# Kernel optimization log

Measured on AMD Instinct MI355X. Metric: run time of the kernel, lower is better.

Reference implementation:

```python
import jax, jax.numpy as jnp
import numpy as np

NODE_TYPE_SIZE = 9      # common.NodeType.SIZE in MeshGraphNets
N_NODES = 1_000_000
N_CELLS = 2_000_000


def setup_inputs() -> dict:
    key = jax.random.key(0)
    k1, k2, k3, k4, k5 = jax.random.split(key, 5)
    world_pos = jax.random.normal(k1, (1, N_NODES, 3), dtype=jnp.float32)
    prev_world_pos = world_pos + 0.01 * jax.random.normal(k2, (1, N_NODES, 3), dtype=jnp.float32)
    mesh_pos = jax.random.normal(k3, (1, N_NODES, 3), dtype=jnp.float32)
    node_type = jax.random.randint(k4, (1, N_NODES, 1), 0, NODE_TYPE_SIZE, dtype=jnp.int64)
    # random triangles with guaranteed-distinct vertices (avoids degenerate
    # zero-length edges, matching real meshes where triangle corners differ)
    base = jax.random.randint(k5, (N_CELLS, 1), 0, N_NODES, dtype=jnp.int64)
    cells = jnp.mod(base + jnp.arange(3, dtype=jnp.int64)[None, :], N_NODES)[None]
    return {
        'world_pos': world_pos,
        'prev_world_pos': prev_world_pos,
        'mesh_pos': mesh_pos,
        'node_type': node_type,
        'cells': cells,
    }


def _triangles_to_edges(cells):
    # cells: [F, 3] -> bidirectional directed edge list [2 * 3F]
    a, b, c = cells[:, 0], cells[:, 1], cells[:, 2]
    u = jnp.concatenate([a, b, c])  # edge endpoints (a,b),(b,c),(c,a)
    v = jnp.concatenate([b, c, a])
    senders = jnp.concatenate([u, v])
    receivers = jnp.concatenate([v, u])
    return senders, receivers


def reference(world_pos, prev_world_pos, mesh_pos, node_type, cells):
    # squeeze the leading batch dim of 1, as the torch module does
    world_pos = jnp.squeeze(world_pos, 0)          # [N, 3]
    prev_world_pos = jnp.squeeze(prev_world_pos, 0)
    mesh_pos = jnp.squeeze(mesh_pos, 0)
    node_type = jnp.squeeze(node_type, 0)          # [N, 1]
    cells = jnp.squeeze(cells, 0)                  # [F, 3]

    velocity = world_pos - prev_world_pos                                   # [N, 3]
    nt_onehot = jax.nn.one_hot(node_type[:, 0], NODE_TYPE_SIZE,
                               dtype=world_pos.dtype)                        # [N, 9]
    node_features = jnp.concatenate([velocity, nt_onehot], axis=-1)          # [N, 12]

    senders, receivers = _triangles_to_edges(cells)                          # [E]
    rel_world = world_pos[senders] - world_pos[receivers]                    # [E, 3]
    rel_mesh = mesh_pos[senders] - mesh_pos[receivers]                       # [E, 3]
    edge_features = jnp.concatenate([
        rel_world,
        jnp.linalg.norm(rel_world, axis=-1, keepdims=True),
        rel_mesh,
        jnp.linalg.norm(rel_mesh, axis=-1, keepdims=True),
    ], axis=-1)                                                              # [E, 7]
    return node_features, edge_features
```

## Files before the change

### kernel.cpp

```cpp
#include <hip/hip_runtime.h>

__global__ void node_kernel(const float* __restrict__ w,
                            const float* __restrict__ p,
                            const int* __restrict__ nt,
                            float4* __restrict__ out, int n_nodes) {
    int i = blockIdx.x * blockDim.x + threadIdx.x;
    if (i >= n_nodes) return;
    size_t b = 3 * (size_t)i;
    float v0 = w[b + 0] - p[b + 0];
    float v1 = w[b + 1] - p[b + 1];
    float v2 = w[b + 2] - p[b + 2];
    int t = nt[i];
    float4 f0 = make_float4(v0, v1, v2, t == 0 ? 1.f : 0.f);
    float4 f1 = make_float4(t == 1 ? 1.f : 0.f, t == 2 ? 1.f : 0.f,
                            t == 3 ? 1.f : 0.f, t == 4 ? 1.f : 0.f);
    float4 f2 = make_float4(t == 5 ? 1.f : 0.f, t == 6 ? 1.f : 0.f,
                            t == 7 ? 1.f : 0.f, t == 8 ? 1.f : 0.f);
    float4* dst = out + 3 * (size_t)i;
    dst[0] = f0;
    dst[1] = f1;
    dst[2] = f2;
}

__device__ __forceinline__ void load3(const float* __restrict__ base, int n,
                                      float& x, float& y, float& z) {
    const float* q = base + 3 * (size_t)n;
    x = q[0]; y = q[1]; z = q[2];
}

__device__ __forceinline__ void emit(float4* __restrict__ ef, size_t e_fwd, size_t e_rev,
                                     float rwx, float rwy, float rwz,
                                     float rmx, float rmy, float rmz) {
    float nw = sqrtf(rwx * rwx + rwy * rwy + rwz * rwz);
    float nm = sqrtf(rmx * rmx + rmy * rmy + rmz * rmz);
    ef[2 * e_fwd + 0] = make_float4(rwx, rwy, rwz, nw);
    ef[2 * e_fwd + 1] = make_float4(rmx, rmy, rmz, nm);
    ef[2 * e_rev + 0] = make_float4(-rwx, -rwy, -rwz, nw);
    ef[2 * e_rev + 1] = make_float4(-rmx, -rmy, -rmz, nm);
}

__global__ void edge_kernel(const float* __restrict__ world,
                            const float* __restrict__ mesh,
                            const int* __restrict__ cells,
                            float4* __restrict__ ef, int n_cells) {
    int c = blockIdx.x * blockDim.x + threadIdx.x;
    if (c >= n_cells) return;
    size_t cb = 3 * (size_t)c;
    int ia = cells[cb + 0];
    int ib = cells[cb + 1];
    int ic = cells[cb + 2];

    float wax, way, waz, wbx, wby, wbz, wcx, wcy, wcz;
    load3(world, ia, wax, way, waz);
    load3(world, ib, wbx, wby, wbz);
    load3(world, ic, wcx, wcy, wcz);
    float max_, may_, maz_, mbx_, mby_, mbz_, mcx_, mcy_, mcz_;
    load3(mesh, ia, max_, may_, maz_);
    load3(mesh, ib, mbx_, mby_, mbz_);
    load3(mesh, ic, mcx_, mcy_, mcz_);

    size_t NC = (size_t)n_cells;
    size_t e = (size_t)c;
    emit(ef, e,          e + 3 * NC,
         wax - wbx, way - wby, waz - wbz,
         max_ - mbx_, may_ - mby_, maz_ - mbz_);
    emit(ef, e + NC,     e + 4 * NC,
         wbx - wcx, wby - wcy, wbz - wcz,
         mbx_ - mcx_, mby_ - mcy_, mbz_ - mcz_);
    emit(ef, e + 2 * NC, e + 5 * NC,
         wcx - wax, wcy - way, wcz - waz,
         mcx_ - max_, mcy_ - may_, mcz_ - maz_);
}

extern "C" void kernel_launch(void* const* d_in, const int* in_sizes, int n_in,
                              void* d_out, int out_size, void* d_ws, size_t ws_size,
                              hipStream_t stream) {
    const float* world = (const float*)d_in[0];
    const float* prev  = (const float*)d_in[1];
    const float* mesh  = (const float*)d_in[2];
    const int* ntype   = (const int*)d_in[3];
    const int* cells   = (const int*)d_in[4];
    int n_nodes = in_sizes[0] / 3;
    int n_cells = in_sizes[4] / 3;

    float* out = (float*)d_out;
    float4* nf = (float4*)out;
    float4* ef = (float4*)(out + (size_t)n_nodes * 12);

    dim3 blk(256);
    dim3 g_node((n_nodes + 255) / 256);
    dim3 g_edge((n_cells + 255) / 256);
    node_kernel<<<g_node, blk, 0, stream>>>(world, prev, ntype, nf, n_nodes);
    edge_kernel<<<g_edge, blk, 0, stream>>>(world, mesh, cells, ef, n_cells);
}
```

Before: 598.7 us.

## Fuse node and edge kernels into one launch with vectorized nontemporal stores

Merges the node and edge kernels into a single grid, with block ranges split between edge and node work, so one launch replaces two and the tail of one can overlap the other. Each edge thread handles two cells and reads cell indices as int2. Each node thread handles four nodes using float4 loads of positions and an int4 load of types. All outputs are written with nontemporal 16-byte stores. It adds more registers per thread, fewer threads in flight for the gather-bound edge work, and tail-handling branches.

Result: slower. 960.0 us (+60.3%).

```diff
diff --git a/kernel.cpp b/kernel.cpp
--- a/kernel.cpp
+++ b/kernel.cpp
@@ -1,75 +1,151 @@
 #include <hip/hip_runtime.h>
 
-__global__ void node_kernel(const float* __restrict__ w,
-                            const float* __restrict__ p,
-                            const int* __restrict__ nt,
-                            float4* __restrict__ out, int n_nodes) {
-    int i = blockIdx.x * blockDim.x + threadIdx.x;
-    if (i >= n_nodes) return;
-    size_t b = 3 * (size_t)i;
-    float v0 = w[b + 0] - p[b + 0];
-    float v1 = w[b + 1] - p[b + 1];
-    float v2 = w[b + 2] - p[b + 2];
-    int t = nt[i];
-    float4 f0 = make_float4(v0, v1, v2, t == 0 ? 1.f : 0.f);
-    float4 f1 = make_float4(t == 1 ? 1.f : 0.f, t == 2 ? 1.f : 0.f,
-                            t == 3 ? 1.f : 0.f, t == 4 ? 1.f : 0.f);
-    float4 f2 = make_float4(t == 5 ? 1.f : 0.f, t == 6 ? 1.f : 0.f,
-                            t == 7 ? 1.f : 0.f, t == 8 ? 1.f : 0.f);
-    float4* dst = out + 3 * (size_t)i;
-    dst[0] = f0;
-    dst[1] = f1;
-    dst[2] = f2;
+typedef float f4 __attribute__((ext_vector_type(4)));
+
+struct F3 { float x, y, z; };
+
+__device__ __forceinline__ F3 ldf3(const float* __restrict__ p) {
+    F3 r;
+    __builtin_memcpy(&r, p, sizeof(F3));
+    return r;
+}
+__device__ __forceinline__ F3 sub3(F3 a, F3 b) { F3 r{a.x - b.x, a.y - b.y, a.z - b.z}; return r; }
+__device__ __forceinline__ float nrm3(F3 v) { return sqrtf(v.x * v.x + v.y * v.y + v.z * v.z); }
+
+__device__ __forceinline__ void stnt4(f4* __restrict__ p, float a, float b, float c, float d) {
+    f4 v; v.x = a; v.y = b; v.z = c; v.w = d;
+    __builtin_nontemporal_store(v, p);
 }
 
-__device__ __forceinline__ void load3(const float* __restrict__ base, int n,
-                                      float& x, float& y, float& z) {
-    const float* q = base + 3 * (size_t)n;
-    x = q[0]; y = q[1]; z = q[2];
+__device__ __forceinline__ void store_pair(f4* __restrict__ ef, size_t fb, size_t rb,
+                                           F3 rw0, float nw0, F3 rm0, float nm0,
+                                           F3 rw1, float nw1, F3 rm1, float nm1) {
+    stnt4(ef + fb + 0,  rw0.x,  rw0.y,  rw0.z, nw0);
+    stnt4(ef + fb + 1,  rm0.x,  rm0.y,  rm0.z, nm0);
+    stnt4(ef + fb + 2,  rw1.x,  rw1.y,  rw1.z, nw1);
+    stnt4(ef + fb + 3,  rm1.x,  rm1.y,  rm1.z, nm1);
+    stnt4(ef + rb + 0, -rw0.x, -rw0.y, -rw0.z, nw0);
+    stnt4(ef + rb + 1, -rm0.x, -rm0.y, -rm0.z, nm0);
+    stnt4(ef + rb + 2, -rw1.x, -rw1.y, -rw1.z, nw1);
+    stnt4(ef + rb + 3, -rm1.x, -rm1.y, -rm1.z, nm1);
 }
 
-__device__ __forceinline__ void emit(float4* __restrict__ ef, size_t e_fwd, size_t e_rev,
-                                     float rwx, float rwy, float rwz,
-                                     float rmx, float rmy, float rmz) {
-    float nw = sqrtf(rwx * rwx + rwy * rwy + rwz * rwz);
-    float nm = sqrtf(rmx * rmx + rmy * rmy + rmz * rmz);
-    ef[2 * e_fwd + 0] = make_float4(rwx, rwy, rwz, nw);
-    ef[2 * e_fwd + 1] = make_float4(rmx, rmy, rmz, nm);
-    ef[2 * e_rev + 0] = make_float4(-rwx, -rwy, -rwz, nw);
-    ef[2 * e_rev + 1] = make_float4(-rmx, -rmy, -rmz, nm);
+__device__ __forceinline__ void node_rows(f4* __restrict__ dst, float vx, float vy, float vz, int t) {
+    stnt4(dst + 0, vx, vy, vz, t == 0 ? 1.f : 0.f);
+    stnt4(dst + 1, t == 1 ? 1.f : 0.f, t == 2 ? 1.f : 0.f, t == 3 ? 1.f : 0.f, t == 4 ? 1.f : 0.f);
+    stnt4(dst + 2, t == 5 ? 1.f : 0.f, t == 6 ? 1.f : 0.f, t == 7 ? 1.f : 0.f, t == 8 ? 1.f : 0.f);
 }
 
-__global__ void edge_kernel(const float* __restrict__ world,
-                            const float* __restrict__ mesh,
-                            const int* __restrict__ cells,
-                            float4* __restrict__ ef, int n_cells) {
-    int c = blockIdx.x * blockDim.x + threadIdx.x;
-    if (c >= n_cells) return;
-    size_t cb = 3 * (size_t)c;
-    int ia = cells[cb + 0];
-    int ib = cells[cb + 1];
-    int ic = cells[cb + 2];
+__device__ __forceinline__ void edge_one(const float* __restrict__ world,
+                                         const float* __restrict__ mesh,
+                                         const int* __restrict__ cells,
+                                         f4* __restrict__ ef, size_t NC, size_t c) {
+    const int* cb = cells + 3 * c;
+    int ia = cb[0], ib = cb[1], ic = cb[2];
+    F3 wa = ldf3(world + 3 * (size_t)ia), wb = ldf3(world + 3 * (size_t)ib), wc = ldf3(world + 3 * (size_t)ic);
+    F3 ma = ldf3(mesh  + 3 * (size_t)ia), mb = ldf3(mesh  + 3 * (size_t)ib), mc = ldf3(mesh  + 3 * (size_t)ic);
+    {
+        F3 rw = sub3(wa, wb), rm = sub3(ma, mb);
+        float nw = nrm3(rw), nm = nrm3(rm);
+        size_t e = c, er = c + 3 * NC;
+        stnt4(ef + 2 * e + 0,  rw.x,  rw.y,  rw.z, nw); stnt4(ef + 2 * e + 1,  rm.x,  rm.y,  rm.z, nm);
+        stnt4(ef + 2 * er + 0, -rw.x, -rw.y, -rw.z, nw); stnt4(ef + 2 * er + 1, -rm.x, -rm.y, -rm.z, nm);
+    }
+    {
+        F3 rw = sub3(wb, wc), rm = sub3(mb, mc);
+        float nw = nrm3(rw), nm = nrm3(rm);
+        size_t e = c + NC, er = c + 4 * NC;
+        stnt4(ef + 2 * e + 0,  rw.x,  rw.y,  rw.z, nw); stnt4(ef + 2 * e + 1,  rm.x,  rm.y,  rm.z, nm);
+        stnt4(ef + 2 * er + 0, -rw.x, -rw.y, -rw.z, nw); stnt4(ef + 2 * er + 1, -rm.x, -rm.y, -rm.z, nm);
+    }
+    {
+        F3 rw = sub3(wc, wa), rm = sub3(mc, ma);
+        float nw = nrm3(rw), nm = nrm3(rm);
+        size_t e = c + 2 * NC, er = c + 5 * NC;
+        stnt4(ef + 2 * e + 0,  rw.x,  rw.y,  rw.z, nw); stnt4(ef + 2 * e + 1,  rm.x,  rm.y,  rm.z, nm);
+        stnt4(ef + 2 * er + 0, -rw.x, -rw.y, -rw.z, nw); stnt4(ef + 2 * er + 1, -rm.x, -rm.y, -rm.z, nm);
+    }
+}
 
-    float wax, way, waz, wbx, wby, wbz, wcx, wcy, wcz;
-    load3(world, ia, wax, way, waz);
-    load3(world, ib, wbx, wby, wbz);
-    load3(world, ic, wcx, wcy, wcz);
-    float max_, may_, maz_, mbx_, mby_, mbz_, mcx_, mcy_, mcz_;
-    load3(mesh, ia, max_, may_, maz_);
-    load3(mesh, ib, mbx_, mby_, mbz_);
-    load3(mesh, ic, mcx_, mcy_, mcz_);
+__global__ void __launch_bounds__(256) fused(const float* __restrict__ world,
+                                             const float* __restrict__ prev,
+                                             const float* __restrict__ mesh,
+                                             const int* __restrict__ ntype,
+                                             const int* __restrict__ cells,
+                                             f4* __restrict__ nf,
+                                             f4* __restrict__ ef,
+                                             int n_nodes, int n_cells, int edge_blocks) {
+    if ((int)blockIdx.x < edge_blocks) {
+        int p = blockIdx.x * 256 + threadIdx.x;
+        int npairs = n_cells >> 1;
+        size_t NC = (size_t)n_cells;
+        if (p < npairs) {
+            const int2* cb = (const int2*)(cells + 6 * (size_t)p);
+            int2 q0 = cb[0], q1 = cb[1], q2 = cb[2];
+            int ia0 = q0.x, ib0 = q0.y, ic0 = q1.x;
+            int ia1 = q1.y, ib1 = q2.x, ic1 = q2.y;
 
-    size_t NC = (size_t)n_cells;
-    size_t e = (size_t)c;
-    emit(ef, e,          e + 3 * NC,
-         wax - wbx, way - wby, waz - wbz,
-         max_ - mbx_, may_ - mby_, maz_ - mbz_);
-    emit(ef, e + NC,     e + 4 * NC,
-         wbx - wcx, wby - wcy, wbz - wcz,
-         mbx_ - mcx_, mby_ - mcy_, mbz_ - mcz_);
-    emit(ef, e + 2 * NC, e + 5 * NC,
-         wcx - wax, wcy - way, wcz - waz,
-         mcx_ - max_, mcy_ - may_, mcz_ - maz_);
+            F3 wa0 = ldf3(world + 3 * (size_t)ia0);
+            F3 wb0 = ldf3(world + 3 * (size_t)ib0);
+            F3 wc0 = ldf3(world + 3 * (size_t)ic0);
+            F3 wa1 = ldf3(world + 3 * (size_t)ia1);
+            F3 wb1 = ldf3(world + 3 * (size_t)ib1);
+            F3 wc1 = ldf3(world + 3 * (size_t)ic1);
+            F3 ma0 = ldf3(mesh + 3 * (size_t)ia0);
+            F3 mb0 = ldf3(mesh + 3 * (size_t)ib0);
+            F3 mc0 = ldf3(mesh + 3 * (size_t)ic0);
+            F3 ma1 = ldf3(mesh + 3 * (size_t)ia1);
+            F3 mb1 = ldf3(mesh + 3 * (size_t)ib1);
+            F3 mc1 = ldf3(mesh + 3 * (size_t)ic1);
+
+            size_t c0 = 2 * (size_t)p;
+            {
+                F3 rw0 = sub3(wa0, wb0), rm0 = sub3(ma0, mb0);
+                F3 rw1 = sub3(wa1, wb1), rm1 = sub3(ma1, mb1);
+                store_pair(ef, 2 * (0 * NC + c0), 2 * (3 * NC + c0),
+                           rw0, nrm3(rw0), rm0, nrm3(rm0), rw1, nrm3(rw1), rm1, nrm3(rm1));
+            }
+            {
+                F3 rw0 = sub3(wb0, wc0), rm0 = sub3(mb0, mc0);
+                F3 rw1 = sub3(wb1, wc1), rm1 = sub3(mb1, mc1);
+                store_pair(ef, 2 * (1 * NC + c0), 2 * (4 * NC + c0),
+                           rw0, nrm3(rw0), rm0, nrm3(rm0), rw1, nrm3(rw1), rm1, nrm3(rm1));
+            }
+            {
+                F3 rw0 = sub3(wc0, wa0), rm0 = sub3(mc0, ma0);
+                F3 rw1 = sub3(wc1, wa1), rm1 = sub3(mc1, ma1);
+                store_pair(ef, 2 * (2 * NC + c0), 2 * (5 * NC + c0),
+                           rw0, nrm3(rw0), rm0, nrm3(rm0), rw1, nrm3(rw1), rm1, nrm3(rm1));
+            }
+        } else if ((n_cells & 1) && p == npairs) {
+            edge_one(world, mesh, cells, ef, NC, (size_t)n_cells - 1);
+        }
+    } else {
+        int t = (blockIdx.x - edge_blocks) * 256 + threadIdx.x;
+        int n4 = n_nodes >> 2;
+        if (t < n4) {
+            const f4* w4 = (const f4*)world + 3 * (size_t)t;
+            const f4* p4 = (const f4*)prev  + 3 * (size_t)t;
+            f4 wv0 = w4[0], wv1 = w4[1], wv2 = w4[2];
+            f4 pv0 = p4[0], pv1 = p4[1], pv2 = p4[2];
+            int4 tt = *((const int4*)ntype + t);
+            f4* dst = nf + 12 * (size_t)t;
+            node_rows(dst + 0, wv0.x - pv0.x, wv0.y - pv0.y, wv0.z - pv0.z, tt.x);
+            node_rows(dst + 3, wv0.w - pv0.w, wv1.x - pv1.x, wv1.y - pv1.y, tt.y);
+            node_rows(dst + 6, wv1.z - pv1.z, wv1.w - pv1.w, wv2.x - pv2.x, tt.z);
+            node_rows(dst + 9, wv2.y - pv2.y, wv2.z - pv2.z, wv2.w - pv2.w, tt.w);
+        } else {
+            int k = t - n4;
+            int n = (n4 << 2) + k;
+            if (n < n_nodes) {
+                size_t b = 3 * (size_t)n;
+                float vx = world[b + 0] - prev[b + 0];
+                float vy = world[b + 1] - prev[b + 1];
+                float vz = world[b + 2] - prev[b + 2];
+                node_rows(nf + 3 * (size_t)n, vx, vy, vz, ntype[n]);
+            }
+        }
+    }
 }
 
 extern "C" void kernel_launch(void* const* d_in, const int* in_sizes, int n_in,
@@ -84,12 +160,16 @@
     int n_cells = in_sizes[4] / 3;
 
     float* out = (float*)d_out;
-    float4* nf = (float4*)out;
-    float4* ef = (float4*)(out + (size_t)n_nodes * 12);
+    f4* nf = (f4*)out;
+    f4* ef = (f4*)(out + (size_t)n_nodes * 12);
 
-    dim3 blk(256);
-    dim3 g_node((n_nodes + 255) / 256);
-    dim3 g_edge((n_cells + 255) / 256);
-    node_kernel<<<g_node, blk, 0, stream>>>(world, prev, ntype, nf, n_nodes);
-    edge_kernel<<<g_edge, blk, 0, stream>>>(world, mesh, cells, ef, n_cells);
+    int npairs = n_cells >> 1;
+    int edge_threads = npairs + (n_cells & 1);
+    int edge_blocks = (edge_threads + 255) / 256;
+    int n4 = n_nodes >> 2;
+    int node_threads = n4 + (n_nodes - (n4 << 2));
+    int node_blocks = (node_threads + 255) / 256;
+
+    fused<<<dim3(edge_blocks + node_blocks), dim3(256), 0, stream>>>(
+        world, prev, mesh, ntype, cells, nf, ef, n_nodes, n_cells, edge_blocks);
 }
```
